# Kernel tuning notes

Measured on AMD Instinct MI355X. Metric: run time of the kernel, lower is better.

The kernel has to match this reference:

```python
import jax, jax.numpy as jnp
import numpy as np
import math

# Shapes: b, coarse nodes, fine cells per coarse cell grouped as (seq_out, seq_in)
B, N_OUT, SO, SI, NV, NC = 4, 10240, 4, 4, 1, 32
N_PHI, N_DIST, N_SIGMA = 4, 4, 1
DIST_UNIT = 2.0  # (global_level_no - global_level_encode) * grid_layer_encode.nh_dist
MIN_SIGMA = 1e-10


def setup_inputs() -> dict:
    key = jax.random.key(0)
    k1, k2, k3 = jax.random.split(key, 3)
    n_in = N_OUT * SO * SI
    # x: (b, n_in, nh_in=1, nv, nc), nh_in_encode=False path (x.unsqueeze(2))
    x = jax.random.normal(k1, (B, n_in, 1, NV, NC), dtype=jnp.float32)
    # relative coordinates (cartesian, rotated frame): (1, n_out, seq_out, seq_in)
    coords_x = jax.random.uniform(k2, (1, N_OUT, SO, SI), dtype=jnp.float32,
                                  minval=-DIST_UNIT, maxval=DIST_UNIT)
    coords_y = jax.random.uniform(k3, (1, N_OUT, SO, SI), dtype=jnp.float32,
                                  minval=-DIST_UNIT, maxval=DIST_UNIT)
    # parameters exactly as in __init__
    phis = jnp.linspace(-jnp.pi, jnp.pi, N_PHI + 1)[:-1].astype(jnp.float32)
    d = jnp.arange(1, 2 * N_DIST, 2, dtype=jnp.float32) / (N_DIST * 2)
    dists_param = -jnp.log(1.0 / d - 1.0)  # inverse-sigmoid init
    s = 1.0 / (2 * N_DIST * math.sqrt(2 * math.log(2)))
    sigma_param = (-math.log(1.0 / s - 1.0)) * jnp.ones((N_SIGMA,), jnp.float32)
    return dict(x=x, coords_x=coords_x, coords_y=coords_y,
                phis=phis, dists_param=dists_param, sigma_param=sigma_param)


def reference(x, coords_x, coords_y, phis, dists_param, sigma_param):
    b = x.shape[0]
    nv, nc = x.shape[-2], x.shape[-1]
    n_out, so, si = coords_x.shape[1], coords_x.shape[2], coords_x.shape[3]

    # get_spatial_weights
    dists = DIST_UNIT * jax.nn.sigmoid(dists_param)              # (D,)
    mu_x = jnp.cos(phis)[:, None] * dists[None, :]               # (P, D)
    mu_y = jnp.sin(phis)[:, None] * dists[None, :]               # (P, D)
    sigma = jnp.maximum(DIST_UNIT * jax.nn.sigmoid(sigma_param), MIN_SIGMA)  # (S,)

    dx = coords_x[0][..., None, None] - mu_x                     # (O, so, si, P, D)
    dy = coords_y[0][..., None, None] - mu_y                     # (O, so, si, P, D)
    w = jnp.exp(-0.5 * (dx * dx + dy * dy)[..., None] / (sigma * sigma))  # (O, so, si, P, D, S)

    # mult_weights_t (n_out <= n_in branch): normalize over the (so, si) receptive field
    w = w / (w.sum(axis=(1, 2), keepdims=True) + 1e-20)

    # grouped view: n_in = n_out * so * si, nh_in = 1
    xr = x.reshape(b, n_out, so, si, nv, nc)
    # weighted reduce over the receptive field against mixture weights
    out = jnp.einsum('boijvc,oijpds->bovpdsc', xr, w)            # (b, O, nv, P, D, S, nc)
    return out
```

## Files before the change

### kernel.cpp

```cpp
#include <hip/hip_runtime.h>
#include <math.h>

namespace {

constexpr int NOUT = 10240;
constexpr int OW   = 4;
constexpr int NB   = 4;
constexpr int NIJ  = 16;
constexpr int NPD  = 16;
constexpr int NC   = 32;
constexpr int NIN  = NOUT * NIJ;
constexpr int WPAD = 20;

typedef float vfloat4 __attribute__((ext_vector_type(4)));

__device__ __forceinline__ void fma4(float4& a, float s, const float4& v) {
    a.x = fmaf(s, v.x, a.x);
    a.y = fmaf(s, v.y, a.y);
    a.z = fmaf(s, v.z, a.z);
    a.w = fmaf(s, v.w, a.w);
}

__device__ __forceinline__ void nt_store4(float4* p, const float4& v) {
    vfloat4 nv = { v.x, v.y, v.z, v.w };
    __builtin_nontemporal_store(nv, reinterpret_cast<vfloat4*>(p));
}

__global__ __launch_bounds__(256) void polnorm_kernel(
    const float* __restrict__ x,
    const float* __restrict__ cx,
    const float* __restrict__ cy,
    const float* __restrict__ phis,
    const float* __restrict__ dists_p,
    const float* __restrict__ sigma_p,
    float* __restrict__ out)
{
    __shared__ __align__(16) float s_w[OW][NPD][WPAD];
    __shared__ __align__(16) float s_x[OW][NIJ * NC];

    const int t   = threadIdx.x;
    const int wid = t >> 6;
    const int l   = t & 63;
    const int c4  = l & 7;
    const int pda = l >> 3;

    const int o = blockIdx.x * OW + wid;

    const float4* xg = reinterpret_cast<const float4*>(x) + (size_t)o * (NIJ * NC / 4);
    float4*       og = reinterpret_cast<float4*>(out)     + (size_t)o * (NPD * NC / 4);
    const size_t xstride = (size_t)NIN * NC / 4;
    const size_t ostride = (size_t)NOUT * NPD * NC / 4;

    float4 x0[NB], x1[NB];
    #pragma unroll
    for (int bi = 0; bi < NB; ++bi) {
        x0[bi] = xg[(size_t)bi * xstride + l];
        x1[bi] = xg[(size_t)bi * xstride + 64 + l];
    }

    float inv0, inv1;
    {
        const int pdf = l >> 2;
        const int ijq = (l & 3) * 4;
        const int p = pdf >> 2, dd = pdf & 3;

        const float dist = 2.0f / (1.0f + expf(-dists_p[dd]));
        const float phi  = phis[p];
        const float mux  = cosf(phi) * dist;
        const float muy  = sinf(phi) * dist;
        float sg = 2.0f / (1.0f + expf(-sigma_p[0]));
        sg = fmaxf(sg, 1e-10f);
        const float coef = -0.5f / (sg * sg);

        const float4 cxi = *reinterpret_cast<const float4*>(&cx[o * NIJ + ijq]);
        const float4 cyi = *reinterpret_cast<const float4*>(&cy[o * NIJ + ijq]);

        float4 w;
        { float dx = cxi.x - mux, dy = cyi.x - muy; w.x = expf(coef * (dx*dx + dy*dy)); }
        { float dx = cxi.y - mux, dy = cyi.y - muy; w.y = expf(coef * (dx*dx + dy*dy)); }
        { float dx = cxi.z - mux, dy = cyi.z - muy; w.z = expf(coef * (dx*dx + dy*dy)); }
        { float dx = cxi.w - mux, dy = cyi.w - muy; w.w = expf(coef * (dx*dx + dy*dy)); }

        float s = w.x + w.y + w.z + w.w;
        s += __shfl_xor(s, 1);
        s += __shfl_xor(s, 2);
        const float inv = 1.0f / (s + 1e-20f);

        *reinterpret_cast<float4*>(&s_w[wid][pdf][ijq]) = w;

        inv0 = __shfl(inv, pda * 4);
        inv1 = __shfl(inv, pda * 4 + 32);
    }

    float4 wa[4], wb[4];
    #pragma unroll
    for (int kk = 0; kk < 4; ++kk) {
        wa[kk] = *reinterpret_cast<const float4*>(&s_w[wid][pda][kk * 4]);
        wb[kk] = *reinterpret_cast<const float4*>(&s_w[wid][pda + 8][kk * 4]);
    }

    float4* xs = reinterpret_cast<float4*>(s_x[wid]);

    #pragma unroll
    for (int bi = 0; bi < NB; ++bi) {
        xs[l] = x0[bi];
        xs[64 + l] = x1[bi];

        float4 acc0 = make_float4(0.f, 0.f, 0.f, 0.f);
        float4 acc1 = make_float4(0.f, 0.f, 0.f, 0.f);

        #pragma unroll
        for (int kk = 0; kk < 4; ++kk) {
            const float4 xv0 = xs[(kk * 4 + 0) * 8 + c4];
            const float4 xv1 = xs[(kk * 4 + 1) * 8 + c4];
            const float4 xv2 = xs[(kk * 4 + 2) * 8 + c4];
            const float4 xv3 = xs[(kk * 4 + 3) * 8 + c4];
            fma4(acc0, wa[kk].x, xv0); fma4(acc1, wb[kk].x, xv0);
            fma4(acc0, wa[kk].y, xv1); fma4(acc1, wb[kk].y, xv1);
            fma4(acc0, wa[kk].z, xv2); fma4(acc1, wb[kk].z, xv2);
            fma4(acc0, wa[kk].w, xv3); fma4(acc1, wb[kk].w, xv3);
        }

        acc0.x *= inv0; acc0.y *= inv0; acc0.z *= inv0; acc0.w *= inv0;
        acc1.x *= inv1; acc1.y *= inv1; acc1.z *= inv1; acc1.w *= inv1;

        nt_store4(&og[(size_t)bi * ostride + l], acc0);
        nt_store4(&og[(size_t)bi * ostride + 64 + l], acc1);
    }
}

}

extern "C" void kernel_launch(void* const* d_in, const int* in_sizes, int n_in,
                              void* d_out, int out_size, void* d_ws, size_t ws_size,
                              hipStream_t stream) {
    const float* x  = (const float*)d_in[0];
    const float* cx = (const float*)d_in[1];
    const float* cy = (const float*)d_in[2];
    const float* ph = (const float*)d_in[3];
    const float* dp = (const float*)d_in[4];
    const float* sp = (const float*)d_in[5];
    float* out = (float*)d_out;

    dim3 grid(NOUT / OW);
    dim3 block(256);
    hipLaunchKernelGGL(polnorm_kernel, grid, block, 0, stream,
                       x, cx, cy, ph, dp, sp, out);
}
```

Measured before the change: 30.89 us.

## Stream x directly into LDS with double-buffered async loads per wave

Measured after the change: 56.97 us. 1.84x slower.

```diff
diff --git a/kernel.cpp b/kernel.cpp
--- a/kernel.cpp
+++ b/kernel.cpp
@@ -1,10 +1,11 @@
 #include <hip/hip_runtime.h>
 #include <math.h>
+#include <stdint.h>
 
 namespace {
 
 constexpr int NOUT = 10240;
-constexpr int OW   = 4;
+constexpr int OW   = 2;
 constexpr int NB   = 4;
 constexpr int NIJ  = 16;
 constexpr int NPD  = 16;
@@ -26,7 +27,17 @@
     __builtin_nontemporal_store(nv, reinterpret_cast<vfloat4*>(p));
 }
 
-__global__ __launch_bounds__(256) void polnorm_kernel(
+__device__ __forceinline__ void gload_lds16(const float4* gsrc, float4* ldst) {
+    __builtin_amdgcn_global_load_lds(
+        (const __attribute__((address_space(1))) uint32_t*)gsrc,
+        (__attribute__((address_space(3))) uint32_t*)ldst, 16, 0, 0);
+}
+
+template <int N> __device__ __forceinline__ void wait_vm() {
+    asm volatile("s_waitcnt vmcnt(%0)" :: "n"(N) : "memory");
+}
+
+__global__ __launch_bounds__(128, 8) void polnorm_kernel(
     const float* __restrict__ x,
     const float* __restrict__ cx,
     const float* __restrict__ cy,
@@ -35,8 +46,8 @@
     const float* __restrict__ sigma_p,
     float* __restrict__ out)
 {
+    __shared__ __align__(16) float s_x[OW][2][NIJ * NC];
     __shared__ __align__(16) float s_w[OW][NPD][WPAD];
-    __shared__ __align__(16) float s_x[OW][NIJ * NC];
 
     const int t   = threadIdx.x;
     const int wid = t >> 6;
@@ -51,19 +62,22 @@
     const size_t xstride = (size_t)NIN * NC / 4;
     const size_t ostride = (size_t)NOUT * NPD * NC / 4;
 
-    float4 x0[NB], x1[NB];
-    #pragma unroll
-    for (int bi = 0; bi < NB; ++bi) {
-        x0[bi] = xg[(size_t)bi * xstride + l];
-        x1[bi] = xg[(size_t)bi * xstride + 64 + l];
-    }
+    const int pdf = l >> 2;
+    const int ijq = (l & 3) * 4;
+    const float4 cxi = *reinterpret_cast<const float4*>(&cx[o * NIJ + ijq]);
+    const float4 cyi = *reinterpret_cast<const float4*>(&cy[o * NIJ + ijq]);
+
+    float4* xb0 = reinterpret_cast<float4*>(s_x[wid][0]);
+    float4* xb1 = reinterpret_cast<float4*>(s_x[wid][1]);
+
+    gload_lds16(xg + l,            xb0);
+    gload_lds16(xg + 64 + l,       xb0 + 64);
+    gload_lds16(xg + xstride + l,      xb1);
+    gload_lds16(xg + xstride + 64 + l, xb1 + 64);
 
     float inv0, inv1;
     {
-        const int pdf = l >> 2;
-        const int ijq = (l & 3) * 4;
         const int p = pdf >> 2, dd = pdf & 3;
-
         const float dist = 2.0f / (1.0f + expf(-dists_p[dd]));
         const float phi  = phis[p];
         const float mux  = cosf(phi) * dist;
@@ -71,9 +85,6 @@
         float sg = 2.0f / (1.0f + expf(-sigma_p[0]));
         sg = fmaxf(sg, 1e-10f);
         const float coef = -0.5f / (sg * sg);
-
-        const float4 cxi = *reinterpret_cast<const float4*>(&cx[o * NIJ + ijq]);
-        const float4 cyi = *reinterpret_cast<const float4*>(&cy[o * NIJ + ijq]);
 
         float4 w;
         { float dx = cxi.x - mux, dy = cyi.x - muy; w.x = expf(coef * (dx*dx + dy*dy)); }
@@ -87,7 +98,6 @@
         const float inv = 1.0f / (s + 1e-20f);
 
         *reinterpret_cast<float4*>(&s_w[wid][pdf][ijq]) = w;
-
         inv0 = __shfl(inv, pda * 4);
         inv1 = __shfl(inv, pda * 4 + 32);
     }
@@ -99,34 +109,37 @@
         wb[kk] = *reinterpret_cast<const float4*>(&s_w[wid][pda + 8][kk * 4]);
     }
 
-    float4* xs = reinterpret_cast<float4*>(s_x[wid]);
+#define TILE_BODY(BI, BUF, DO_RESTAGE, RESTAGE_BI, WAITN)                        \
+    {                                                                            \
+        wait_vm<WAITN>();                                                        \
+        float4 acc0 = make_float4(0.f, 0.f, 0.f, 0.f);                           \
+        float4 acc1 = make_float4(0.f, 0.f, 0.f, 0.f);                           \
+        _Pragma("unroll")                                                        \
+        for (int kk = 0; kk < 4; ++kk) {                                         \
+            const float4 xv0 = (BUF)[(kk * 4 + 0) * 8 + c4];                     \
+            const float4 xv1 = (BUF)[(kk * 4 + 1) * 8 + c4];                     \
+            const float4 xv2 = (BUF)[(kk * 4 + 2) * 8 + c4];                     \
+            const float4 xv3 = (BUF)[(kk * 4 + 3) * 8 + c4];                     \
+            fma4(acc0, wa[kk].x, xv0); fma4(acc1, wb[kk].x, xv0);                \
+            fma4(acc0, wa[kk].y, xv1); fma4(acc1, wb[kk].y, xv1);                \
+            fma4(acc0, wa[kk].z, xv2); fma4(acc1, wb[kk].z, xv2);                \
+            fma4(acc0, wa[kk].w, xv3); fma4(acc1, wb[kk].w, xv3);                \
+        }                                                                        \
+        acc0.x *= inv0; acc0.y *= inv0; acc0.z *= inv0; acc0.w *= inv0;          \
+        acc1.x *= inv1; acc1.y *= inv1; acc1.z *= inv1; acc1.w *= inv1;          \
+        nt_store4(&og[(size_t)(BI) * ostride + l], acc0);                        \
+        nt_store4(&og[(size_t)(BI) * ostride + 64 + l], acc1);                   \
+        if (DO_RESTAGE) {                                                        \
+            gload_lds16(xg + (size_t)(RESTAGE_BI) * xstride + l,      (BUF));    \
+            gload_lds16(xg + (size_t)(RESTAGE_BI) * xstride + 64 + l, (BUF)+64); \
+        }                                                                        \
+    }
 
-    #pragma unroll
-    for (int bi = 0; bi < NB; ++bi) {
-        xs[l] = x0[bi];
-        xs[64 + l] = x1[bi];
-
-        float4 acc0 = make_float4(0.f, 0.f, 0.f, 0.f);
-        float4 acc1 = make_float4(0.f, 0.f, 0.f, 0.f);
-
-        #pragma unroll
-        for (int kk = 0; kk < 4; ++kk) {
-            const float4 xv0 = xs[(kk * 4 + 0) * 8 + c4];
-            const float4 xv1 = xs[(kk * 4 + 1) * 8 + c4];
-            const float4 xv2 = xs[(kk * 4 + 2) * 8 + c4];
-            const float4 xv3 = xs[(kk * 4 + 3) * 8 + c4];
-            fma4(acc0, wa[kk].x, xv0); fma4(acc1, wb[kk].x, xv0);
-            fma4(acc0, wa[kk].y, xv1); fma4(acc1, wb[kk].y, xv1);
-            fma4(acc0, wa[kk].z, xv2); fma4(acc1, wb[kk].z, xv2);
-            fma4(acc0, wa[kk].w, xv3); fma4(acc1, wb[kk].w, xv3);
-        }
-
-        acc0.x *= inv0; acc0.y *= inv0; acc0.z *= inv0; acc0.w *= inv0;
-        acc1.x *= inv1; acc1.y *= inv1; acc1.z *= inv1; acc1.w *= inv1;
-
-        nt_store4(&og[(size_t)bi * ostride + l], acc0);
-        nt_store4(&og[(size_t)bi * ostride + 64 + l], acc1);
-    }
+    TILE_BODY(0, xb0, true, 2, 2)
+    TILE_BODY(1, xb1, true, 3, 4)
+    TILE_BODY(2, xb0, false, 0, 4)
+    TILE_BODY(3, xb1, false, 0, 2)
+#undef TILE_BODY
 }
 
 }
@@ -143,7 +156,7 @@
     float* out = (float*)d_out;
 
     dim3 grid(NOUT / OW);
-    dim3 block(256);
+    dim3 block(128);
     hipLaunchKernelGGL(polnorm_kernel, grid, block, 0, stream,
                        x, cx, cy, ph, dp, sp, out);
 }
```
